# Performance work log

Measured on AMD Instinct MI355X. Metric: run time of the kernel, lower is better.

## Reference

```python
import jax, jax.numpy as jnp
import numpy as np

DIM = 1024
HEADS = 16
HEAD_DIM = DIM // HEADS
FFN = 4 * DIM
EPS = 1e-5


def layer_norm(x, g, b):
    mu = jnp.mean(x, axis=-1, keepdims=True)
    var = jnp.mean(jnp.square(x - mu), axis=-1, keepdims=True)
    return (x - mu) * jax.lax.rsqrt(var + EPS) * g + b


def setup_inputs() -> dict:
    key = jax.random.key(0)
    ks = jax.random.split(key, 12)
    s_d = 1.0 / np.sqrt(DIM)
    s_f = 1.0 / np.sqrt(FFN)
    return {
        "x": jax.random.normal(ks[0], (2, 2048, DIM), dtype=jnp.float32),
        "ln1_g": jnp.ones((DIM,), jnp.float32),
        "ln1_b": jnp.zeros((DIM,), jnp.float32),
        "q_w": jax.random.normal(ks[1], (DIM, DIM), jnp.float32) * s_d,
        "k_w": jax.random.normal(ks[2], (DIM, DIM), jnp.float32) * s_d,
        "v_w": jax.random.normal(ks[3], (DIM, DIM), jnp.float32) * s_d,
        "o_w": jax.random.normal(ks[4], (DIM, DIM), jnp.float32) * s_d,
        "ln2_g": jnp.ones((DIM,), jnp.float32),
        "ln2_b": jnp.zeros((DIM,), jnp.float32),
        "ffn_in_w": jax.random.normal(ks[5], (FFN, DIM), jnp.float32) * s_d,
        "ffn_in_b": jnp.zeros((FFN,), jnp.float32),
        "sw_w": jax.random.normal(ks[6], (FFN, FFN), jnp.float32) * s_f,
        "sw_v": jax.random.normal(ks[7], (FFN, FFN), jnp.float32) * s_f,
        "ffn_out_w": jax.random.normal(ks[8], (DIM, FFN), jnp.float32) * s_f,
        "ffn_out_b": jnp.zeros((DIM,), jnp.float32),
    }


def reference(x, ln1_g, ln1_b, q_w, k_w, v_w, o_w, ln2_g, ln2_b,
              ffn_in_w, ffn_in_b, sw_w, sw_v, ffn_out_w, ffn_out_b):
    B, L, D = x.shape
    scale = HEAD_DIM ** -0.5

    # --- attention block ---
    h = layer_norm(x, ln1_g, ln1_b)
    q = (h @ q_w.T).reshape(B, L, HEADS, HEAD_DIM).transpose(0, 2, 1, 3)
    k = (h @ k_w.T).reshape(B, L, HEADS, HEAD_DIM).transpose(0, 2, 1, 3)
    v = (h @ v_w.T).reshape(B, L, HEADS, HEAD_DIM).transpose(0, 2, 1, 3)
    attn = jnp.einsum("bhqd,bhkd->bhqk", q, k) * scale
    attn = jax.nn.softmax(attn, axis=-1)
    out = jnp.einsum("bhqk,bhkd->bhqd", attn, v)
    out = out.transpose(0, 2, 1, 3).reshape(B, L, D)
    x = x + out @ o_w.T

    # --- FFN block: Linear -> SwiGLU -> Linear ---
    h = layer_norm(x, ln2_g, ln2_b)
    u = h @ ffn_in_w.T + ffn_in_b                 # [B,L,FFN]
    g = jax.nn.silu(u @ sw_w.T) * (u @ sw_v.T)    # SwiGLU
    x = x + g @ ffn_out_w.T + ffn_out_b
    return x
```

## Files before the change

kernel.cpp:

```cpp
#include <hip/hip_runtime.h>
#include <hip/hip_bf16.h>

#define TOK 4096
#define DIM 1024
#define FFN_N 4096
#define SEQ 2048
#define HD 64
#define QKS 3072

using short8 = __attribute__((ext_vector_type(8))) short;
using short4v = __attribute__((ext_vector_type(4))) short;
using f32x4 = __attribute__((ext_vector_type(4))) float;

__device__ __forceinline__ short f2b(float f){
  return __builtin_bit_cast(short, __float2bfloat16(f));
}
__device__ __forceinline__ float b2f(short s){
  return __bfloat162float(__builtin_bit_cast(__hip_bfloat16, s));
}
__device__ __forceinline__ unsigned cvtpk(float lo, float hi){
  unsigned r;
  asm("v_cvt_pk_bf16_f32 %0, %1, %2" : "=v"(r) : "v"(lo), "v"(hi));
  return r;
}

__device__ __forceinline__ void gl_lds16(const short* g, short* l){
  __builtin_amdgcn_global_load_lds(
      (const __attribute__((address_space(1))) unsigned int*)g,
      (__attribute__((address_space(3))) unsigned int*)l, 16, 0, 0);
}

#define BARRAW() asm volatile("s_barrier" ::: "memory")
#define VMCNT(n) asm volatile("s_waitcnt vmcnt(" #n ")" ::: "memory")

__global__ __launch_bounds__(256) void castk(const float* __restrict__ src,
                                             short* __restrict__ dst, int n){
  int stride = gridDim.x*256*4;
  for (int i = (blockIdx.x*256 + threadIdx.x)*4; i < n; i += stride){
    float4 v = *reinterpret_cast<const float4*>(src + i);
    short4v o; o[0]=f2b(v.x); o[1]=f2b(v.y); o[2]=f2b(v.z); o[3]=f2b(v.w);
    *reinterpret_cast<short4v*>(dst + i) = o;
  }
}

__global__ __launch_bounds__(256) void lnk(const float* __restrict__ x,
                                           const float* __restrict__ g,
                                           const float* __restrict__ b,
                                           short* __restrict__ out){
  int row = blockIdx.x;
  int t = threadIdx.x;
  const float* xr = x + (size_t)row*DIM;
  float4 v = *reinterpret_cast<const float4*>(xr + t*4);
  float s = v.x+v.y+v.z+v.w;
  float s2 = v.x*v.x+v.y*v.y+v.z*v.z+v.w*v.w;
  #pragma unroll
  for (int off=1; off<64; off<<=1){ s += __shfl_xor(s,off); s2 += __shfl_xor(s2,off); }
  __shared__ float as_[4], as2_[4];
  if ((t&63)==0){ as_[t>>6]=s; as2_[t>>6]=s2; }
  __syncthreads();
  s = as_[0]+as_[1]+as_[2]+as_[3];
  s2 = as2_[0]+as2_[1]+as2_[2]+as2_[3];
  float mu = s * (1.0f/DIM);
  float var = s2 * (1.0f/DIM) - mu*mu;
  float r = rsqrtf(var + 1e-5f);
  float4 gv = *reinterpret_cast<const float4*>(g + t*4);
  float4 bv = *reinterpret_cast<const float4*>(b + t*4);
  short4v o;
  o[0]=f2b((v.x-mu)*r*gv.x + bv.x);
  o[1]=f2b((v.y-mu)*r*gv.y + bv.y);
  o[2]=f2b((v.z-mu)*r*gv.z + bv.z);
  o[3]=f2b((v.w-mu)*r*gv.w + bv.w);
  *reinterpret_cast<short4v*>(out + (size_t)row*DIM + t*4) = o;
}

template<int MODE>
__global__ __launch_bounds__(256,2) void gemm_bt(
    const short* __restrict__ A, const short* __restrict__ Bt,
    short* __restrict__ Cb, float* __restrict__ Cf,
    const float* __restrict__ bias, const float* __restrict__ resid,
    const short* __restrict__ aux,
    int M, int N, int K)
{
  __shared__ __align__(16) short Al[128*32];
  __shared__ __align__(16) short Bl[128*32];
  const int tid = threadIdx.x, lane = tid & 63, w = tid >> 6;
  const int wr = w >> 1, wc = w & 1;
  const int bx = blockIdx.x, by = blockIdx.y;

  const short* ga0 = A  + (size_t)(by*128 + w*32 + (lane>>2))*K + (lane&3)*8;
  const short* gb0 = Bt + (size_t)(bx*128 + w*32 + (lane>>2))*K + (lane&3)*8;
  short* la0 = &Al[w*32*32];
  short* lb0 = &Bl[w*32*32];

  f32x4 acc[4][4] = {};

  for (int k0 = 0; k0 < K; k0 += 32){
    __syncthreads();
    gl_lds16(ga0 + k0,                 la0);
    gl_lds16(ga0 + k0 + (size_t)16*K,  la0 + 16*32);
    gl_lds16(gb0 + k0,                 lb0);
    gl_lds16(gb0 + k0 + (size_t)16*K,  lb0 + 16*32);
    __syncthreads();
    short8 af[4], bf[4];
    #pragma unroll
    for (int m=0;m<4;m++)
      af[m] = *reinterpret_cast<const short8*>(&Al[(wr*64 + m*16 + (lane&15))*32 + (lane>>4)*8]);
    #pragma unroll
    for (int n=0;n<4;n++)
      bf[n] = *reinterpret_cast<const short8*>(&Bl[(wc*64 + n*16 + (lane&15))*32 + (lane>>4)*8]);
    #pragma unroll
    for (int m=0;m<4;m++)
      #pragma unroll
      for (int n=0;n<4;n++)
        acc[m][n] = __builtin_amdgcn_mfma_f32_16x16x32_bf16(af[m], bf[n], acc[m][n], 0,0,0);
  }

  #pragma unroll
  for (int m=0;m<4;m++){
    #pragma unroll
    for (int n=0;n<4;n++){
      #pragma unroll
      for (int j=0;j<4;j++){
        int r = by*128 + wr*64 + m*16 + ((lane>>4)<<2) + j;
        int c = bx*128 + wc*64 + n*16 + (lane&15);
        float v = acc[m][n][j];
        if (MODE==1 || MODE==3) v += bias[c];
        size_t idx = (size_t)r*N + c;
        if (MODE==4){
          float a = b2f(aux[idx]);
          float sg = a / (1.0f + __expf(-a));
          Cb[idx] = f2b(sg * v);
        } else if (MODE<=1) {
          Cb[idx] = f2b(v);
        } else {
          Cf[idx] = resid[idx] + v;
        }
      }
    }
  }
}

template<int MODE>
__global__ __launch_bounds__(512,2) void gemm256(
    const short* __restrict__ A, const short* __restrict__ Bt,
    short* __restrict__ Cb,
    const float* __restrict__ bias, const short* __restrict__ aux,
    int M, int N, int K)
{
  __shared__ __align__(16) short L[65536];
  const int tid = threadIdx.x, lane = tid&63, w = tid>>6;
  const int q15 = lane&15, h8 = lane>>4;
  const int wm = w>>2, wn = w&3;
  const int NT = K>>6;

  int bid = blockIdx.x;
  int wg = (bid&7)*(gridDim.x>>3) + (bid>>3);
  const int by = wg >> 4, bx = wg & 15;

  const int isub = w*8 + (lane>>3);
  const int koff = ((lane&7) ^ ((lane>>3)&7))*8;

  const short* gA[2][2]; const short* gB[2][2];
  #pragma unroll
  for (int hh=0; hh<2; hh++){
    #pragma unroll
    for (int j=0; j<2; j++){
      int i = j*64 + isub;
      int Ra = by*256 + (i>>6)*128 + hh*64 + (i&63);
      gA[hh][j] = A + (size_t)Ra*K + koff;
      int Rb = bx*256 + (i>>5)*64 + hh*32 + (i&31);
      gB[hh][j] = Bt + (size_t)Rb*K + koff;
    }
  }

  auto stA = [&](int db, int hh, int j, int kt){
    gl_lds16(gA[hh][j] + (size_t)kt*64, &L[db*32768 + hh*8192 + j*4096 + w*512]);
  };
  auto stB = [&](int db, int hh, int j, int kt){
    gl_lds16(gB[hh][j] + (size_t)kt*64, &L[db*32768 + (2+hh)*8192 + j*4096 + w*512]);
  };
  auto rdA = [&](int db, int mh, int m, int ks)->short8{
    int i = wm*64 + m*16 + q15;
    int ch = (ks*4 + h8) ^ (i&7);
    return *reinterpret_cast<const short8*>(&L[db*32768 + mh*8192 + i*64 + ch*8]);
  };
  auto rdB = [&](int db, int nh, int n, int ks)->short8{
    int i = wn*32 + n*16 + q15;
    int ch = (ks*4 + h8) ^ (i&7);
    return *reinterpret_cast<const short8*>(&L[db*32768 + (2+nh)*8192 + i*64 + ch*8]);
  };

  f32x4 acc[8][4] = {};
  short8 af[4][2], bf0[2][2], bf1[2][2];

#define MFMA_QUAD(MH, NH, BF)                                                  \
  __builtin_amdgcn_s_setprio(1);                                               \
  _Pragma("unroll")                                                            \
  for (int m=0;m<4;m++){                                                       \
    _Pragma("unroll")                                                          \
    for (int n=0;n<2;n++){                                                     \
      acc[(MH)*4+m][(NH)*2+n] = __builtin_amdgcn_mfma_f32_16x16x32_bf16(       \
          af[m][0], BF[n][0], acc[(MH)*4+m][(NH)*2+n], 0,0,0);                 \
      acc[(MH)*4+m][(NH)*2+n] = __builtin_amdgcn_mfma_f32_16x16x32_bf16(       \
          af[m][1], BF[n][1], acc[(MH)*4+m][(NH)*2+n], 0,0,0);                 \
    }                                                                          \
  }                                                                            \
  __builtin_amdgcn_s_setprio(0);

  stA(0,0,0,0); stA(0,0,1,0);
  stB(0,0,0,0); stB(0,0,1,0);
  stA(0,1,0,0); stA(0,1,1,0);
  stB(0,1,0,0); stB(0,1,1,0);
  VMCNT(4);
  BARRAW();

  for (int t = 0; t < NT; ++t){
    const int db = t&1;
    const bool pf = (t+1 < NT);

    #pragma unroll
    for (int m=0;m<4;m++){ af[m][0]=rdA(db,0,m,0); af[m][1]=rdA(db,0,m,1); }
    #pragma unroll
    for (int n=0;n<2;n++){ bf0[n][0]=rdB(db,0,n,0); bf0[n][1]=rdB(db,0,n,1); }
    if (pf){ stA(db^1,0,0,t+1); stA(db^1,0,1,t+1);
             stB(db^1,0,0,t+1); stB(db^1,0,1,t+1); }
    MFMA_QUAD(0,0,bf0);

    if (pf){ VMCNT(4); } else { VMCNT(0); }
    BARRAW();

    #pragma unroll
    for (int n=0;n<2;n++){ bf1[n][0]=rdB(db,1,n,0); bf1[n][1]=rdB(db,1,n,1); }
    if (pf){ stA(db^1,1,0,t+1); stA(db^1,1,1,t+1);
             stB(db^1,1,0,t+1); stB(db^1,1,1,t+1); }
    MFMA_QUAD(0,1,bf1);

    #pragma unroll
    for (int m=0;m<4;m++){ af[m][0]=rdA(db,1,m,0); af[m][1]=rdA(db,1,m,1); }
    MFMA_QUAD(1,1,bf1);
    MFMA_QUAD(1,0,bf0);

    if (pf){ VMCNT(4); }
    BARRAW();
  }

  #pragma unroll
  for (int mq=0;mq<8;mq++){
    #pragma unroll
    for (int nq=0;nq<4;nq++){
      #pragma unroll
      for (int jj=0;jj<4;jj++){
        int r = by*256 + wm*128 + mq*16 + h8*4 + jj;
        int c = bx*256 + wn*64  + nq*16 + q15;
        float v = acc[mq][nq][jj];
        if (MODE==1) v += bias[c];
        size_t idx = (size_t)r*N + c;
        if (MODE==4){
          float a = b2f(aux[idx]);
          float sg = a / (1.0f + __expf(-a));
          Cb[idx] = f2b(sg * v);
        } else {
          Cb[idx] = f2b(v);
        }
      }
    }
  }
#undef MFMA_QUAD
}

__global__ __launch_bounds__(256) void vtrk(const short* __restrict__ V,
                                            short* __restrict__ Vt){
  __shared__ __align__(16) short T[64*72];
  const int tid = threadIdx.x;
  const int bh = blockIdx.y;
  const int b = bh >> 4, hd = bh & 15;
  const int t0 = blockIdx.x * 64;
  const short* src = V + (size_t)b*SEQ*QKS + (size_t)hd*HD;

  const int r = tid>>2, c = tid&3;
  short8 a0 = *reinterpret_cast<const short8*>(src + (size_t)(t0+r)*QKS + c*8);
  short8 a1 = *reinterpret_cast<const short8*>(src + (size_t)(t0+r)*QKS + (c+4)*8);
  *reinterpret_cast<short8*>(&T[r*72 + c*8]) = a0;
  *reinterpret_cast<short8*>(&T[r*72 + (c+4)*8]) = a1;
  __syncthreads();

  short* dst = Vt + (size_t)bh*HD*SEQ;
  #pragma unroll
  for (int dd=0; dd<2; dd++){
    int d = (tid>>3) + dd*32;
    int tc = tid&7;
    short8 o;
    #pragma unroll
    for (int j=0;j<8;j++) o[j] = T[(tc*8+j)*72 + d];
    *reinterpret_cast<short8*>(dst + (size_t)d*SEQ + t0 + tc*8) = o;
  }
}

__global__ __launch_bounds__(512) void attnk(
    const short* __restrict__ Q, const short* __restrict__ K,
    const short* __restrict__ Vt, short* __restrict__ O)
{
  __shared__ __align__(16) short Kl[64*64];
  __shared__ __align__(16) short Vl[64*64];
  __shared__ __align__(16) short Pl[8*16*72];

  const int tid = threadIdx.x, lane = tid&63, w = tid>>6;
  const int h = lane>>4, q15 = lane&15;
  const int bh = blockIdx.y;
  const int b = bh >> 4, hd = bh & 15;
  const int q0 = blockIdx.x * 128;
  const size_t base  = (size_t)b*SEQ*QKS + (size_t)hd*HD;
  const size_t obase = (size_t)b*SEQ*DIM + (size_t)hd*HD;
  const size_t vbase = (size_t)bh*HD*SEQ;

  short8 aq[2];
  {
    int qrow = q0 + w*16 + q15;
    const short* qp = Q + base + (size_t)qrow*QKS + h*8;
    aq[0] = *reinterpret_cast<const short8*>(qp);
    aq[1] = *reinterpret_cast<const short8*>(qp + 32);
  }

  float mrun = -1e30f, lrun = 0.f;
  f32x4 o[4] = {};

  const int srow = lane>>3;
  const int schunk = (lane&7) ^ srow;
  const short* kg = K  + base  + (size_t)(w*8 + srow)*QKS + schunk*8;
  const short* vg = Vt + vbase + (size_t)(w*8 + srow)*SEQ + schunk*8;
  short* kl = &Kl[(w*8)*64];
  short* vl = &Vl[(w*8)*64];

  short* plw = &Pl[w*16*72];
  const int xk = (q15&7);

  for (int kv0 = 0; kv0 < SEQ; kv0 += 64){
    __syncthreads();
    gl_lds16(kg + (size_t)kv0*QKS, kl);
    gl_lds16(vg + kv0, vl);
    __syncthreads();

    f32x4 s[4];
    #pragma unroll
    for (int nt=0; nt<4; nt++){
      const short8 kf0 = *reinterpret_cast<const short8*>(
          &Kl[(nt*16+q15)*64 + ((h    ^ xk)*8)]);
      const short8 kf1 = *reinterpret_cast<const short8*>(
          &Kl[(nt*16+q15)*64 + (((4+h)^ xk)*8)]);
      f32x4 t = {};
      t = __builtin_amdgcn_mfma_f32_16x16x32_bf16(kf0, aq[0], t, 0,0,0);
      t = __builtin_amdgcn_mfma_f32_16x16x32_bf16(kf1, aq[1], t, 0,0,0);
      s[nt] = t * 0.125f;
    }

    float pm = s[0][0];
    #pragma unroll
    for (int nt=0; nt<4; nt++)
      #pragma unroll
      for (int j=0; j<4; j++) pm = fmaxf(pm, s[nt][j]);
    pm = fmaxf(pm, __shfl_xor(pm, 16));
    pm = fmaxf(pm, __shfl_xor(pm, 32));

    float mn = fmaxf(mrun, pm);
    float al = __expf(mrun - mn);
    mrun = mn;
    float rs = 0.f;
    #pragma unroll
    for (int nt=0; nt<4; nt++)
      #pragma unroll
      for (int j=0; j<4; j++){
        s[nt][j] = __expf(s[nt][j] - mn);
        rs += s[nt][j];
      }
    rs += __shfl_xor(rs, 16);
    rs += __shfl_xor(rs, 32);
    lrun = lrun*al + rs;

    float alj[4];
    #pragma unroll
    for (int j=0;j<4;j++) alj[j] = __shfl(al, 4*h + j);
    #pragma unroll
    for (int dt=0;dt<4;dt++)
      #pragma unroll
      for (int j=0;j<4;j++) o[dt][j] *= alj[j];

    #pragma unroll
    for (int nt=0;nt<4;nt++){
      uint2 u;
      u.x = cvtpk(s[nt][0], s[nt][1]);
      u.y = cvtpk(s[nt][2], s[nt][3]);
      *reinterpret_cast<uint2*>(&plw[q15*72 + nt*16 + 4*h]) = u;
    }
    asm volatile("s_waitcnt lgkmcnt(0)" ::: "memory");
    const short8 ap0 = *reinterpret_cast<const short8*>(&plw[q15*72 +      h*8]);
    const short8 ap1 = *reinterpret_cast<const short8*>(&plw[q15*72 + 32 + h*8]);

    #pragma unroll
    for (int dt=0;dt<4;dt++){
      const short8 vf0 = *reinterpret_cast<const short8*>(
          &Vl[(dt*16+q15)*64 + ((h    ^ xk)*8)]);
      const short8 vf1 = *reinterpret_cast<const short8*>(
          &Vl[(dt*16+q15)*64 + (((4+h)^ xk)*8)]);
      o[dt] = __builtin_amdgcn_mfma_f32_16x16x32_bf16(ap0, vf0, o[dt], 0,0,0);
      o[dt] = __builtin_amdgcn_mfma_f32_16x16x32_bf16(ap1, vf1, o[dt], 0,0,0);
    }
  }

  float rl[4];
  #pragma unroll
  for (int j=0;j<4;j++) rl[j] = 1.0f / __shfl(lrun, 4*h + j);
  #pragma unroll
  for (int dt=0;dt<4;dt++)
    #pragma unroll
    for (int j=0;j<4;j++){
      int qrow = q0 + w*16 + 4*h + j;
      O[obase + (size_t)qrow*DIM + dt*16 + q15] = f2b(o[dt][j]*rl[j]);
    }
}

extern "C" void kernel_launch(void* const* d_in, const int* in_sizes, int n_in,
                              void* d_out, int out_size, void* d_ws, size_t ws_size,
                              hipStream_t stream) {
  const float* x     = (const float*)d_in[0];
  const float* ln1_g = (const float*)d_in[1];
  const float* ln1_b = (const float*)d_in[2];
  const float* q_w   = (const float*)d_in[3];
  const float* k_w   = (const float*)d_in[4];
  const float* v_w   = (const float*)d_in[5];
  const float* o_w   = (const float*)d_in[6];
  const float* ln2_g = (const float*)d_in[7];
  const float* ln2_b = (const float*)d_in[8];
  const float* fi_w  = (const float*)d_in[9];
  const float* fi_b  = (const float*)d_in[10];
  const float* sw_w  = (const float*)d_in[11];
  const float* sw_v  = (const float*)d_in[12];
  const float* fo_w  = (const float*)d_in[13];
  const float* fo_b  = (const float*)d_in[14];
  float* out = (float*)d_out;

  char* W = (char*)d_ws;
  const size_t MB = 1024*1024;
  short* qkvw = (short*)(W +   0*MB);
  short* ow   = (short*)(W +   6*MB);
  short* fiw  = (short*)(W +   8*MB);
  short* sww  = (short*)(W +  16*MB);
  short* swv  = (short*)(W +  48*MB);
  short* fow  = (short*)(W +  80*MB);
  short* hb   = (short*)(W +  88*MB);
  short* qkv  = (short*)(W +  96*MB);
  short* ab   = (short*)(W + 120*MB);
  float* x2   = (float*)(W + 128*MB);
  short* ub   = (short*)(W + 144*MB);
  short* gb   = (short*)(W + 176*MB);
  short* a1   = (short*)(W +  96*MB);
  short* vt   = (short*)(W + 144*MB);

  dim3 blk(256);
  castk<<<1024,blk,0,stream>>>(q_w, qkvw,             1024*1024);
  castk<<<1024,blk,0,stream>>>(k_w, qkvw + 1024*1024, 1024*1024);
  castk<<<1024,blk,0,stream>>>(v_w, qkvw + 2048*1024, 1024*1024);
  castk<<<1024,blk,0,stream>>>(o_w, ow, 1024*1024);
  castk<<<2048,blk,0,stream>>>(fi_w, fiw, 4096*1024);
  castk<<<2048,blk,0,stream>>>(sw_w, sww, 4096*4096);
  castk<<<2048,blk,0,stream>>>(sw_v, swv, 4096*4096);
  castk<<<2048,blk,0,stream>>>(fo_w, fow, 1024*4096);

  lnk<<<TOK,blk,0,stream>>>(x, ln1_g, ln1_b, hb);
  gemm_bt<0><<<dim3(24,32),blk,0,stream>>>(hb, qkvw, qkv, nullptr, nullptr, nullptr, nullptr, TOK, QKS, DIM);
  vtrk<<<dim3(SEQ/64,32),blk,0,stream>>>(qkv + 2048, vt);
  attnk<<<dim3(SEQ/128,32), 512, 0, stream>>>(qkv, qkv + 1024, vt, ab);
  gemm_bt<2><<<dim3(8,32),blk,0,stream>>>(ab, ow, nullptr, x2, nullptr, x, nullptr, TOK, DIM, DIM);
  lnk<<<TOK,blk,0,stream>>>(x2, ln2_g, ln2_b, hb);
  gemm256<1><<<256, 512, 0, stream>>>(hb, fiw, ub, fi_b, nullptr, TOK, FFN_N, DIM);
  gemm256<0><<<256, 512, 0, stream>>>(ub, sww, a1, nullptr, nullptr, TOK, FFN_N, FFN_N);
  gemm256<4><<<256, 512, 0, stream>>>(ub, swv, gb, nullptr, a1, TOK, FFN_N, FFN_N);
  gemm_bt<3><<<dim3(8,32),blk,0,stream>>>(gb, fow, nullptr, out, fo_b, x2, nullptr, TOK, DIM, FFN_N);
}
```

Before: 561.8 us.

## Merge weight casts into one launch and widen attention KV tile with lazy rescale

Replaces the eight weight-cast launches with a single batched kernel that takes a job table indexed by blockIdx.y, removing per-launch overhead. The attention kernel now stages 128 keys/values per iteration instead of 64, which halves the barrier and global-to-LDS round trips, and it only rescales the running max and output accumulators when the new block max exceeds the old one by more than 8. The lazy rescale lets exponentials grow as large as e^8 before correction, trading exactness guarantees for fewer rescale operations. The cast grid is now 512x8 blocks, so the large 16M-element casts get fewer blocks each than before.

```diff
diff --git a/kernel.cpp b/kernel.cpp
--- a/kernel.cpp
+++ b/kernel.cpp
@@ -33,8 +33,16 @@
 #define BARRAW() asm volatile("s_barrier" ::: "memory")
 #define VMCNT(n) asm volatile("s_waitcnt vmcnt(" #n ")" ::: "memory")
 
-__global__ __launch_bounds__(256) void castk(const float* __restrict__ src,
-                                             short* __restrict__ dst, int n){
+struct CastJobs {
+  const float* s[8];
+  short* d[8];
+  int n[8];
+};
+__global__ __launch_bounds__(256) void megacast(CastJobs j){
+  const int t = blockIdx.y;
+  const float* __restrict__ src = j.s[t];
+  short* __restrict__ dst = j.d[t];
+  const int n = j.n[t];
   int stride = gridDim.x*256*4;
   for (int i = (blockIdx.x*256 + threadIdx.x)*4; i < n; i += stride){
     float4 v = *reinterpret_cast<const float4*>(src + i);
@@ -300,8 +308,8 @@
     const short* __restrict__ Q, const short* __restrict__ K,
     const short* __restrict__ Vt, short* __restrict__ O)
 {
-  __shared__ __align__(16) short Kl[64*64];
-  __shared__ __align__(16) short Vl[64*64];
+  __shared__ __align__(16) short Kl[128*64];
+  __shared__ __align__(16) short Vl[64*128];
   __shared__ __align__(16) short Pl[8*16*72];
 
   const int tid = threadIdx.x, lane = tid&63, w = tid>>6;
@@ -324,85 +332,110 @@
   float mrun = -1e30f, lrun = 0.f;
   f32x4 o[4] = {};
 
-  const int srow = lane>>3;
-  const int schunk = (lane&7) ^ srow;
-  const short* kg = K  + base  + (size_t)(w*8 + srow)*QKS + schunk*8;
-  const short* vg = Vt + vbase + (size_t)(w*8 + srow)*SEQ + schunk*8;
-  short* kl = &Kl[(w*8)*64];
-  short* vl = &Vl[(w*8)*64];
+  const int krow = lane>>3;
+  const int kchunk = (lane&7) ^ krow;
+  const short* kg0 = K + base + (size_t)(w*16 + krow)*QKS + kchunk*8;
+  const short* kg1 = kg0 + (size_t)8*QKS;
+  short* kl0 = &Kl[(w*16)*64];
+  short* kl1 = &Kl[(w*16 + 8)*64];
+
+  const int vr = lane>>4;
+  const int vsub = (lane>>3)&1;
+  const int vc7 = lane&7;
+  const short* vg0 = Vt + vbase + (size_t)(w*8 + vr)*SEQ
+                       + vsub*64 + ((vc7 ^ vr)*8);
+  const short* vg1 = Vt + vbase + (size_t)(w*8 + 4 + vr)*SEQ
+                       + vsub*64 + ((vc7 ^ (vr+4))*8);
+  short* vl0 = &Vl[(w*8)*128];
+  short* vl1 = &Vl[(w*8 + 4)*128];
 
   short* plw = &Pl[w*16*72];
   const int xk = (q15&7);
 
-  for (int kv0 = 0; kv0 < SEQ; kv0 += 64){
+  for (int kv0 = 0; kv0 < SEQ; kv0 += 128){
     __syncthreads();
-    gl_lds16(kg + (size_t)kv0*QKS, kl);
-    gl_lds16(vg + kv0, vl);
+    gl_lds16(kg0 + (size_t)kv0*QKS, kl0);
+    gl_lds16(kg1 + (size_t)kv0*QKS, kl1);
+    gl_lds16(vg0 + kv0, vl0);
+    gl_lds16(vg1 + kv0, vl1);
     __syncthreads();
 
-    f32x4 s[4];
-    #pragma unroll
-    for (int nt=0; nt<4; nt++){
-      const short8 kf0 = *reinterpret_cast<const short8*>(
-          &Kl[(nt*16+q15)*64 + ((h    ^ xk)*8)]);
-      const short8 kf1 = *reinterpret_cast<const short8*>(
-          &Kl[(nt*16+q15)*64 + (((4+h)^ xk)*8)]);
-      f32x4 t = {};
-      t = __builtin_amdgcn_mfma_f32_16x16x32_bf16(kf0, aq[0], t, 0,0,0);
-      t = __builtin_amdgcn_mfma_f32_16x16x32_bf16(kf1, aq[1], t, 0,0,0);
-      s[nt] = t * 0.125f;
-    }
-
-    float pm = s[0][0];
-    #pragma unroll
-    for (int nt=0; nt<4; nt++)
-      #pragma unroll
-      for (int j=0; j<4; j++) pm = fmaxf(pm, s[nt][j]);
+    f32x4 s[2][4];
+    #pragma unroll
+    for (int sub=0; sub<2; sub++){
+      #pragma unroll
+      for (int nt=0; nt<4; nt++){
+        const short8 kf0 = *reinterpret_cast<const short8*>(
+            &Kl[(sub*64 + nt*16 + q15)*64 + ((h    ^ xk)*8)]);
+        const short8 kf1 = *reinterpret_cast<const short8*>(
+            &Kl[(sub*64 + nt*16 + q15)*64 + (((4+h)^ xk)*8)]);
+        f32x4 t = {};
+        t = __builtin_amdgcn_mfma_f32_16x16x32_bf16(kf0, aq[0], t, 0,0,0);
+        t = __builtin_amdgcn_mfma_f32_16x16x32_bf16(kf1, aq[1], t, 0,0,0);
+        s[sub][nt] = t * 0.125f;
+      }
+    }
+
+    float pm = s[0][0][0];
+    #pragma unroll
+    for (int sub=0; sub<2; sub++)
+      #pragma unroll
+      for (int nt=0; nt<4; nt++)
+        #pragma unroll
+        for (int j=0; j<4; j++) pm = fmaxf(pm, s[sub][nt][j]);
     pm = fmaxf(pm, __shfl_xor(pm, 16));
     pm = fmaxf(pm, __shfl_xor(pm, 32));
 
-    float mn = fmaxf(mrun, pm);
-    float al = __expf(mrun - mn);
-    mrun = mn;
+    if (!__all(pm - mrun <= 8.0f)){
+      float mn = fmaxf(mrun, pm);
+      float al = __expf(mrun - mn);
+      mrun = mn;
+      lrun *= al;
+      float alj[4];
+      #pragma unroll
+      for (int j=0;j<4;j++) alj[j] = __shfl(al, 4*h + j);
+      #pragma unroll
+      for (int dt=0;dt<4;dt++)
+        #pragma unroll
+        for (int j=0;j<4;j++) o[dt][j] *= alj[j];
+    }
+
     float rs = 0.f;
     #pragma unroll
-    for (int nt=0; nt<4; nt++)
-      #pragma unroll
-      for (int j=0; j<4; j++){
-        s[nt][j] = __expf(s[nt][j] - mn);
-        rs += s[nt][j];
-      }
+    for (int sub=0; sub<2; sub++)
+      #pragma unroll
+      for (int nt=0; nt<4; nt++)
+        #pragma unroll
+        for (int j=0; j<4; j++){
+          s[sub][nt][j] = __expf(s[sub][nt][j] - mrun);
+          rs += s[sub][nt][j];
+        }
     rs += __shfl_xor(rs, 16);
     rs += __shfl_xor(rs, 32);
-    lrun = lrun*al + rs;
-
-    float alj[4];
-    #pragma unroll
-    for (int j=0;j<4;j++) alj[j] = __shfl(al, 4*h + j);
-    #pragma unroll
-    for (int dt=0;dt<4;dt++)
-      #pragma unroll
-      for (int j=0;j<4;j++) o[dt][j] *= alj[j];
-
-    #pragma unroll
-    for (int nt=0;nt<4;nt++){
-      uint2 u;
-      u.x = cvtpk(s[nt][0], s[nt][1]);
-      u.y = cvtpk(s[nt][2], s[nt][3]);
-      *reinterpret_cast<uint2*>(&plw[q15*72 + nt*16 + 4*h]) = u;
-    }
-    asm volatile("s_waitcnt lgkmcnt(0)" ::: "memory");
-    const short8 ap0 = *reinterpret_cast<const short8*>(&plw[q15*72 +      h*8]);
-    const short8 ap1 = *reinterpret_cast<const short8*>(&plw[q15*72 + 32 + h*8]);
-
-    #pragma unroll
-    for (int dt=0;dt<4;dt++){
-      const short8 vf0 = *reinterpret_cast<const short8*>(
-          &Vl[(dt*16+q15)*64 + ((h    ^ xk)*8)]);
-      const short8 vf1 = *reinterpret_cast<const short8*>(
-          &Vl[(dt*16+q15)*64 + (((4+h)^ xk)*8)]);
-      o[dt] = __builtin_amdgcn_mfma_f32_16x16x32_bf16(ap0, vf0, o[dt], 0,0,0);
-      o[dt] = __builtin_amdgcn_mfma_f32_16x16x32_bf16(ap1, vf1, o[dt], 0,0,0);
+    lrun += rs;
+
+    #pragma unroll
+    for (int sub=0; sub<2; sub++){
+      #pragma unroll
+      for (int nt=0;nt<4;nt++){
+        uint2 u;
+        u.x = cvtpk(s[sub][nt][0], s[sub][nt][1]);
+        u.y = cvtpk(s[sub][nt][2], s[sub][nt][3]);
+        *reinterpret_cast<uint2*>(&plw[q15*72 + nt*16 + 4*h]) = u;
+      }
+      asm volatile("s_waitcnt lgkmcnt(0)" ::: "memory");
+      const short8 ap0 = *reinterpret_cast<const short8*>(&plw[q15*72 +      h*8]);
+      const short8 ap1 = *reinterpret_cast<const short8*>(&plw[q15*72 + 32 + h*8]);
+
+      #pragma unroll
+      for (int dt=0;dt<4;dt++){
+        const short8 vf0 = *reinterpret_cast<const short8*>(
+            &Vl[(dt*16+q15)*128 + sub*64 + ((h    ^ xk)*8)]);
+        const short8 vf1 = *reinterpret_cast<const short8*>(
+            &Vl[(dt*16+q15)*128 + sub*64 + (((4+h)^ xk)*8)]);
+        o[dt] = __builtin_amdgcn_mfma_f32_16x16x32_bf16(ap0, vf0, o[dt], 0,0,0);
+        o[dt] = __builtin_amdgcn_mfma_f32_16x16x32_bf16(ap1, vf1, o[dt], 0,0,0);
+      }
     }
   }
 
@@ -456,14 +489,17 @@
   short* vt   = (short*)(W + 144*MB);
 
   dim3 blk(256);
-  castk<<<1024,blk,0,stream>>>(q_w, qkvw,             1024*1024);
-  castk<<<1024,blk,0,stream>>>(k_w, qkvw + 1024*1024, 1024*1024);
-  castk<<<1024,blk,0,stream>>>(v_w, qkvw + 2048*1024, 1024*1024);
-  castk<<<1024,blk,0,stream>>>(o_w, ow, 1024*1024);
-  castk<<<2048,blk,0,stream>>>(fi_w, fiw, 4096*1024);
-  castk<<<2048,blk,0,stream>>>(sw_w, sww, 4096*4096);
-  castk<<<2048,blk,0,stream>>>(sw_v, swv, 4096*4096);
-  castk<<<2048,blk,0,stream>>>(fo_w, fow, 1024*4096);
+
+  CastJobs cj;
+  cj.s[0]=q_w;  cj.d[0]=qkvw;              cj.n[0]=1024*1024;
+  cj.s[1]=k_w;  cj.d[1]=qkvw + 1024*1024;  cj.n[1]=1024*1024;
+  cj.s[2]=v_w;  cj.d[2]=qkvw + 2048*1024;  cj.n[2]=1024*1024;
+  cj.s[3]=o_w;  cj.d[3]=ow;                cj.n[3]=1024*1024;
+  cj.s[4]=fi_w; cj.d[4]=fiw;               cj.n[4]=4096*1024;
+  cj.s[5]=sw_w; cj.d[5]=sww;               cj.n[5]=4096*4096;
+  cj.s[6]=sw_v; cj.d[6]=swv;               cj.n[6]=4096*4096;
+  cj.s[7]=fo_w; cj.d[7]=fow;               cj.n[7]=1024*4096;
+  megacast<<<dim3(512,8),blk,0,stream>>>(cj);
 
   lnk<<<TOK,blk,0,stream>>>(x, ln1_g, ln1_b, hb);
   gemm_bt<0><<<dim3(24,32),blk,0,stream>>>(hb, qkvw, qkv, nullptr, nullptr, nullptr, nullptr, TOK, QKS, DIM);
```

Result: slower. 581.9 us (+3.6%).
